# Performance work log

Measured on AMD Instinct MI355X. Metric: run time of the kernel, lower is better.

The kernel has to match this reference:

```python
import jax, jax.numpy as jnp
import numpy as np

T, B, D, H, O = 512, 64, 256, 1024, 64
DT = 0.1
TAU_MIN, TAU_MAX = 0.01, 1.0
DZDT_MAX, Z_MAX = 10.0, 100.0


def setup_inputs() -> dict:
    key = jax.random.key(0)
    ks = jax.random.split(key, 9)
    sc = lambda k, shape, s: (jax.random.normal(k, shape, jnp.float32) * s)
    return {
        "x": jax.random.normal(ks[0], (T, B, D), jnp.float32),
        # recurrent weights (torch Linear stores [out, in]; y = x @ W.T)
        "W_real": sc(ks[1], (H, H), 0.03),
        "W_imag": sc(ks[2], (H, H), 0.03),
        "U_w": sc(ks[3], (H, D), 0.06),
        "U_b": jnp.zeros((H,), jnp.float32),
        "W_tau_w": sc(ks[4], (H, H), 0.01),
        "W_tau_b": jnp.zeros((H,), jnp.float32),
        # sparse mask logits (module applies sigmoid to these params at fwd time)
        "mask_real": jax.random.normal(ks[5], (H, H), jnp.float32),
        "mask_imag": jax.random.normal(ks[6], (H, H), jnp.float32),
        "tau_bias": jnp.zeros((H,), jnp.float32),
        "b_real": jnp.zeros((H,), jnp.float32),
        "b_imag": jnp.zeros((H,), jnp.float32),
        "out_w": sc(ks[7], (O, H), 0.03),
        "out_b": jnp.zeros((O,), jnp.float32),
    }


def reference(x, W_real, W_imag, U_w, U_b, W_tau_w, W_tau_b,
              mask_real, mask_imag, tau_bias, b_real, b_imag, out_w, out_b):
    # Masked recurrent weights are constant over time: fold sigmoid(mask) once.
    Wr = W_real * jax.nn.sigmoid(mask_real)  # [H,H]
    Wi = W_imag * jax.nn.sigmoid(mask_imag)  # [H,H]
    # Input drive U(x_t) is the same for real and imag parts; precompute for all t.
    Ux = jnp.einsum('tbd,hd->tbh', x, U_w) + U_b  # [T,B,H]

    def step(z, ux):
        zr, zi = z  # complex state as (real, imag), each [B,H]
        dz_r = -zr + jnp.tanh(zr) @ Wr.T + ux + b_real
        dz_i = -zi + jnp.tanh(zi) @ Wi.T + ux + b_imag
        # tau gate from |z| (1e-20 keeps sqrt grad finite at z=0, value unchanged)
        z_mod = jnp.sqrt(zr * zr + zi * zi + 1e-20)
        tau = jax.nn.sigmoid(z_mod @ W_tau_w.T + W_tau_b) + tau_bias
        tau = jnp.clip(tau, TAU_MIN, TAU_MAX) + 1e-6
        dzr = jnp.clip(dz_r / tau, -DZDT_MAX, DZDT_MAX)
        dzi = jnp.clip(dz_i / tau, -DZDT_MAX, DZDT_MAX)
        zr = jnp.clip(zr + DT * dzr, -Z_MAX, Z_MAX)
        zi = jnp.clip(zi + DT * dzi, -Z_MAX, Z_MAX)
        y = zr @ out_w.T + out_b  # readout on real part, [B,O]
        return (zr, zi), y

    z0 = (jnp.zeros((B, H), x.dtype), jnp.zeros((B, H), x.dtype))
    _, ys = jax.lax.scan(step, z0, Ux)
    return ys  # [T,B,O]
```

## Files before the change

### kernel.cpp

```cpp
#include <hip/hip_runtime.h>

static constexpr int TT = 512, BBATCH = 64, DD = 256, HH = 1024, OOUT = 64;

typedef float f32x4 __attribute__((ext_vector_type(4)));
typedef short bfrag __attribute__((ext_vector_type(8)));

__device__ __forceinline__ float sigm(float x) { return 1.0f / (1.0f + __expf(-x)); }
__device__ __forceinline__ float tanh_fast(float x) {
    return 1.0f - 2.0f / (__expf(2.0f * x) + 1.0f);
}
__device__ __forceinline__ unsigned short f2bf(float f) {
    unsigned int u = __builtin_bit_cast(unsigned int, f);
    u += 0x7FFFu + ((u >> 16) & 1u);
    return (unsigned short)(u >> 16);
}

struct Params {
    const float *x, *W_real, *W_imag, *U_w, *U_b, *W_tau_w, *W_tau_b,
                *mask_real, *mask_imag, *tau_bias, *b_real, *b_imag, *out_w, *out_b;
    float* out;
    unsigned short* act;
    float* zread;
    unsigned int* bar;
};

#define LDC(v_, p_, o_) asm volatile("global_load_dwordx4 %0, %1, off offset:" #o_ " sc0 sc1" \
                                     : "=v"(v_) : "v"(p_))
#define WAITV(n_) do { asm volatile("s_waitcnt vmcnt(" #n_ ")" ::: "memory"); \
                       __builtin_amdgcn_sched_barrier(0); } while (0)
#define MFMA(a_, b_, c_) __builtin_amdgcn_mfma_f32_16x16x32_bf16(a_, b_, c_, 0, 0, 0)
#define STC(p_, v_) __hip_atomic_store((p_), (v_), __ATOMIC_RELAXED, __HIP_MEMORY_SCOPE_AGENT)

__global__ void __launch_bounds__(512, 2) lnn_fused(Params p) {
    extern __shared__ char smem[];
    unsigned short* Wlds = (unsigned short*)smem;
    unsigned short* Ulds = (unsigned short*)(smem + 3 * 16 * 1024 * 2);
    float* EX = (float*)(smem + 3 * 16 * 1024 * 2 + 16 * 256 * 2);

    const int tid = threadIdx.x;
    const int wave = tid >> 6, lane = tid & 63;
    const int g = blockIdx.x;
    const int grp = (g & 7) >> 1;
    const int slot = ((g >> 3) << 1) | (g & 1);
    const int h0 = slot * 16, b0 = grp * 16;
    const int ro_b0 = b0 + (slot & 3) * 4, ro_o0 = (slot >> 2) * 4;

    for (int i = tid; i < 3 * 16 * 1024; i += 512) {
        const int mat = i >> 14, r = (i >> 10) & 15, k = i & 1023;
        const int idx = (h0 + r) * HH + k;
        float w;
        if (mat == 0)      w = p.W_real[idx] * sigm(p.mask_real[idx]);
        else if (mat == 1) w = p.W_imag[idx] * sigm(p.mask_imag[idx]);
        else               w = p.W_tau_w[idx];
        const int gk = (k >> 3) ^ (r & 7);
        Wlds[(mat * 16 + r) * 1024 + gk * 8 + (k & 7)] = f2bf(w);
    }
    for (int i = tid; i < 16 * 256; i += 512) {
        const int r = i >> 8, k = i & 255;
        const int gk = (k >> 3) ^ (r & 7);
        Ulds[r * 256 + gk * 8 + (k & 7)] = f2bf(p.U_w[(h0 + r) * DD + k]);
    }

    float zr = 0.f, zi = 0.f, cbr = 0.f, cbi = 0.f, cwtb = 0.f, ctb = 0.f, cub = 0.f;
    int myoff = 0;
    if (tid < 256) {
        const int myb = b0 + (tid >> 4), myh = h0 + (tid & 15);
        myoff = myb * HH + myh;
        cbr = p.b_real[myh]; cbi = p.b_imag[myh];
        cwtb = p.W_tau_b[myh]; ctb = p.tau_bias[myh]; cub = p.U_b[myh];
        STC(p.act + (0 * 2 + 1) * BBATCH * HH + myoff, (unsigned short)0);
        STC(p.act + (1 * 2 + 1) * BBATCH * HH + myoff, (unsigned short)0);
        STC(p.act + (2 * 2 + 1) * BBATCH * HH + myoff, (unsigned short)0);
    }

    unsigned int* bar = p.bar + grp * 32;
    auto group_barrier = [&](unsigned int gen) {
        __syncthreads();
        if (tid == 0) {
            __hip_atomic_fetch_add(bar, 1u, __ATOMIC_RELAXED, __HIP_MEMORY_SCOPE_AGENT);
            const unsigned int tgt = 64u * gen;
            int guard = 1 << 20;
            while (__hip_atomic_load(bar, __ATOMIC_RELAXED, __HIP_MEMORY_SCOPE_AGENT) < tgt
                   && --guard)
                __builtin_amdgcn_s_sleep(1);
        }
        __syncthreads();
    };

    group_barrier(1);

    for (int t = 0; t <= TT; ++t) {
        const int rp = (t + 1) & 1;
        const int wp2 = t & 1;

        if (t < TT && wave < 6) {
            const int mat = wave >> 1, half = wave & 1;
            const int m = lane & 15, kb = lane >> 4, sw = m & 7;
            const unsigned short* aptr = p.act + (mat * 2 + rp) * BBATCH * HH
                                         + (b0 + m) * HH + half * 512 + kb * 8;
            bfrag a0,a1,a2,a3,a4,a5,a6,a7,a8,a9,a10,a11,a12,a13,a14,a15;
            LDC(a0,aptr,0);    LDC(a1,aptr,64);   LDC(a2,aptr,128);  LDC(a3,aptr,192);
            LDC(a4,aptr,256);  LDC(a5,aptr,320);  LDC(a6,aptr,384);  LDC(a7,aptr,448);
            LDC(a8,aptr,512);  LDC(a9,aptr,576);  LDC(a10,aptr,640); LDC(a11,aptr,704);
            LDC(a12,aptr,768); LDC(a13,aptr,832); LDC(a14,aptr,896); LDC(a15,aptr,960);
            f32x4 acc = {0.f, 0.f, 0.f, 0.f};
            const unsigned short* wrow = Wlds + (mat * 16 + m) * 1024;
            #define STW(ks_, av_) acc = MFMA(av_, *(const bfrag*)(wrow + \
                ((((half << 6) + ((ks_) << 2) + kb) ^ sw) << 3)), acc);
            WAITV(8);
            STW(0,a0) STW(1,a1) STW(2,a2) STW(3,a3)
            STW(4,a4) STW(5,a5) STW(6,a6) STW(7,a7)
            WAITV(0);
            STW(8,a8) STW(9,a9) STW(10,a10) STW(11,a11)
            STW(12,a12) STW(13,a13) STW(14,a14) STW(15,a15)
            #undef STW
            #pragma unroll
            for (int q = 0; q < 4; ++q)
                EX[wave * 256 + (kb * 4 + q) * 16 + m] = acc[q];
        } else if (wave == 6 && t < TT) {
            const int m = lane & 15, kb = lane >> 4, sw = m & 7;
            const float* xrow = p.x + ((size_t)t * BBATCH + (b0 + m)) * DD;
            const unsigned short* urow = Ulds + m * 256;
            f32x4 acc = {0.f, 0.f, 0.f, 0.f};
            #pragma unroll
            for (int ks = 0; ks < 8; ++ks) {
                const int k = ks * 32 + kb * 8;
                const f32x4 x0 = *(const f32x4*)(xrow + k);
                const f32x4 x1 = *(const f32x4*)(xrow + k + 4);
                bfrag a;
                a[0]=(short)f2bf(x0[0]); a[1]=(short)f2bf(x0[1]);
                a[2]=(short)f2bf(x0[2]); a[3]=(short)f2bf(x0[3]);
                a[4]=(short)f2bf(x1[0]); a[5]=(short)f2bf(x1[1]);
                a[6]=(short)f2bf(x1[2]); a[7]=(short)f2bf(x1[3]);
                const bfrag b = *(const bfrag*)(urow + (((ks * 4 + kb) ^ sw) << 3));
                acc = MFMA(a, b, acc);
            }
            #pragma unroll
            for (int q = 0; q < 4; ++q)
                EX[6 * 256 + (kb * 4 + q) * 16 + m] = acc[q];
        } else if (wave == 7 && t >= 1) {
            const int r = lane & 15, kq = lane >> 4;
            const int bb = ro_b0 + (r >> 2), oo = ro_o0 + (r & 3);
            const float* zp = p.zread + ((t - 1) & 1) * BBATCH * HH + bb * HH + kq * 256;
            const float* owp = p.out_w + oo * HH + kq * 256;
            float acc = 0.f;
            #define RB(bt_) { \
                const float* zq = zp + (bt_) * 64; \
                f32x4 z0,z1,z2,z3,z4,z5,z6,z7,z8,z9,z10,z11,z12,z13,z14,z15; \
                LDC(z0,zq,0);    LDC(z1,zq,16);   LDC(z2,zq,32);   LDC(z3,zq,48); \
                LDC(z4,zq,64);   LDC(z5,zq,80);   LDC(z6,zq,96);   LDC(z7,zq,112); \
                LDC(z8,zq,128);  LDC(z9,zq,144);  LDC(z10,zq,160); LDC(z11,zq,176); \
                LDC(z12,zq,192); LDC(z13,zq,208); LDC(z14,zq,224); LDC(z15,zq,240); \
                WAITV(0); \
                const f32x4* wq = (const f32x4*)(owp + (bt_) * 64); \
                acc += z0[0]*wq[0][0]+z0[1]*wq[0][1]+z0[2]*wq[0][2]+z0[3]*wq[0][3]; \
                acc += z1[0]*wq[1][0]+z1[1]*wq[1][1]+z1[2]*wq[1][2]+z1[3]*wq[1][3]; \
                acc += z2[0]*wq[2][0]+z2[1]*wq[2][1]+z2[2]*wq[2][2]+z2[3]*wq[2][3]; \
                acc += z3[0]*wq[3][0]+z3[1]*wq[3][1]+z3[2]*wq[3][2]+z3[3]*wq[3][3]; \
                acc += z4[0]*wq[4][0]+z4[1]*wq[4][1]+z4[2]*wq[4][2]+z4[3]*wq[4][3]; \
                acc += z5[0]*wq[5][0]+z5[1]*wq[5][1]+z5[2]*wq[5][2]+z5[3]*wq[5][3]; \
                acc += z6[0]*wq[6][0]+z6[1]*wq[6][1]+z6[2]*wq[6][2]+z6[3]*wq[6][3]; \
                acc += z7[0]*wq[7][0]+z7[1]*wq[7][1]+z7[2]*wq[7][2]+z7[3]*wq[7][3]; \
                acc += z8[0]*wq[8][0]+z8[1]*wq[8][1]+z8[2]*wq[8][2]+z8[3]*wq[8][3]; \
                acc += z9[0]*wq[9][0]+z9[1]*wq[9][1]+z9[2]*wq[9][2]+z9[3]*wq[9][3]; \
                acc += z10[0]*wq[10][0]+z10[1]*wq[10][1]+z10[2]*wq[10][2]+z10[3]*wq[10][3]; \
                acc += z11[0]*wq[11][0]+z11[1]*wq[11][1]+z11[2]*wq[11][2]+z11[3]*wq[11][3]; \
                acc += z12[0]*wq[12][0]+z12[1]*wq[12][1]+z12[2]*wq[12][2]+z12[3]*wq[12][3]; \
                acc += z13[0]*wq[13][0]+z13[1]*wq[13][1]+z13[2]*wq[13][2]+z13[3]*wq[13][3]; \
                acc += z14[0]*wq[14][0]+z14[1]*wq[14][1]+z14[2]*wq[14][2]+z14[3]*wq[14][3]; \
                acc += z15[0]*wq[15][0]+z15[1]*wq[15][1]+z15[2]*wq[15][2]+z15[3]*wq[15][3]; }
            RB(0) RB(1) RB(2) RB(3)
            #undef RB
            acc += __shfl_xor(acc, 16, 64);
            acc += __shfl_xor(acc, 32, 64);
            if (kq == 0)
                p.out[(size_t)(t - 1) * BBATCH * OOUT + bb * OOUT + oo] = acc + p.out_b[oo];
        }

        __syncthreads();

        if (t < TT && tid < 256) {
            const float mr = EX[0 * 256 + tid] + EX[1 * 256 + tid];
            const float mi = EX[2 * 256 + tid] + EX[3 * 256 + tid];
            const float mt = EX[4 * 256 + tid] + EX[5 * 256 + tid];
            const float ux = EX[6 * 256 + tid] + cub;
            const float dr0 = -zr + mr + ux + cbr;
            const float di0 = -zi + mi + ux + cbi;
            float tau = sigm(mt + cwtb) + ctb;
            tau = fminf(fmaxf(tau, 0.01f), 1.0f) + 1e-6f;
            const float dzr = fminf(fmaxf(dr0 / tau, -10.f), 10.f);
            const float dzi = fminf(fmaxf(di0 / tau, -10.f), 10.f);
            zr = fminf(fmaxf(zr + 0.1f * dzr, -100.f), 100.f);
            zi = fminf(fmaxf(zi + 0.1f * dzi, -100.f), 100.f);
            const float ar = tanh_fast(zr), ai = tanh_fast(zi);
            const float zm = sqrtf(zr * zr + zi * zi + 1e-20f);
            STC(p.act + (0 * 2 + wp2) * BBATCH * HH + myoff, f2bf(ar));
            STC(p.act + (1 * 2 + wp2) * BBATCH * HH + myoff, f2bf(ai));
            STC(p.act + (2 * 2 + wp2) * BBATCH * HH + myoff, f2bf(zm));
            STC(p.zread + wp2 * BBATCH * HH + myoff, zr);
        }

        if (t < TT) group_barrier(t + 2);
    }
}

extern "C" void kernel_launch(void* const* d_in, const int* in_sizes, int n_in,
                              void* d_out, int out_size, void* d_ws, size_t ws_size,
                              hipStream_t stream) {
    Params p;
    p.x         = (const float*)d_in[0];
    p.W_real    = (const float*)d_in[1];
    p.W_imag    = (const float*)d_in[2];
    p.U_w       = (const float*)d_in[3];
    p.U_b       = (const float*)d_in[4];
    p.W_tau_w   = (const float*)d_in[5];
    p.W_tau_b   = (const float*)d_in[6];
    p.mask_real = (const float*)d_in[7];
    p.mask_imag = (const float*)d_in[8];
    p.tau_bias  = (const float*)d_in[9];
    p.b_real    = (const float*)d_in[10];
    p.b_imag    = (const float*)d_in[11];
    p.out_w     = (const float*)d_in[12];
    p.out_b     = (const float*)d_in[13];
    p.out   = (float*)d_out;
    p.act   = (unsigned short*)d_ws;
    p.zread = (float*)((char*)d_ws + 786432);
    p.bar   = (unsigned int*)((char*)d_ws + 1310720);

    hipMemsetAsync((char*)d_ws + 1310720, 0, 512, stream);

    constexpr unsigned smem = 3 * 16 * 1024 * 2 + 16 * 256 * 2 + 8 * 256 * 4;
    hipFuncSetAttribute(reinterpret_cast<const void*>(lnn_fused),
                        hipFuncAttributeMaxDynamicSharedMemorySize, smem);
    void* args[] = { &p };
    hipLaunchCooperativeKernel(reinterpret_cast<const void*>(lnn_fused),
                               dim3(256), dim3(512), args, smem, stream);
}
```

Measured before the change: 5.110 ms.

## Add XCD-local partitioned kernel with L2-coherent exchange and fallback path

```diff
diff --git a/kernel.cpp b/kernel.cpp
--- a/kernel.cpp
+++ b/kernel.cpp
@@ -21,17 +21,370 @@
     float* out;
     unsigned short* act;
     float* zread;
-    unsigned int* bar;
+    unsigned int* ctr;
+    unsigned int* xccmap;
+    unsigned short* uslab;
+    unsigned short* wtau;
+    int haveWT;
 };
 
+#define LDL(v_, p_, o_) asm volatile("global_load_dwordx4 %0, %1, off offset:" #o_ " sc0" \
+                                     : "=v"(v_) : "v"(p_))
 #define LDC(v_, p_, o_) asm volatile("global_load_dwordx4 %0, %1, off offset:" #o_ " sc0 sc1" \
+                                     : "=v"(v_) : "v"(p_))
+#define LDP(v_, p_, o_) asm volatile("global_load_dwordx4 %0, %1, off offset:" #o_ \
                                      : "=v"(v_) : "v"(p_))
 #define WAITV(n_) do { asm volatile("s_waitcnt vmcnt(" #n_ ")" ::: "memory"); \
                        __builtin_amdgcn_sched_barrier(0); } while (0)
 #define MFMA(a_, b_, c_) __builtin_amdgcn_mfma_f32_16x16x32_bf16(a_, b_, c_, 0, 0, 0)
 #define STC(p_, v_) __hip_atomic_store((p_), (v_), __ATOMIC_RELAXED, __HIP_MEMORY_SCOPE_AGENT)
 
-__global__ void __launch_bounds__(512, 2) lnn_fused(Params p) {
+#define ISSUE_A16(MACRO_) do { \
+    MACRO_(a0,ap,0);   MACRO_(a1,ap,64);  MACRO_(a2,ap,128);  MACRO_(a3,ap,192);  \
+    MACRO_(a4,ap,256); MACRO_(a5,ap,320); MACRO_(a6,ap,384);  MACRO_(a7,ap,448);  \
+    MACRO_(a8,ap,512); MACRO_(a9,ap,576); MACRO_(a10,ap,640); MACRO_(a11,ap,704); \
+    MACRO_(a12,ap,768);MACRO_(a13,ap,832);MACRO_(a14,ap,896); MACRO_(a15,ap,960); } while (0)
+
+__global__ void __launch_bounds__(512, 2) lnn_xcd(Params p) {
+    extern __shared__ char smem[];
+    unsigned short* Wlds = (unsigned short*)smem;
+    float* EX = (float*)(smem + 131072);
+    __shared__ int sh_mode;
+
+    const int tid = threadIdx.x, wave = tid >> 6, lane = tid & 63;
+    const int g = blockIdx.x, grp = g & 7, slot = g >> 3;
+    const int h0 = slot * 32, b0g = grp * 8;
+    const int gact = grp * 49152;
+    const int gz = grp * 16384;
+
+    for (int i = tid; i < 2 * 32 * 1024; i += 512) {
+        const int mat = i >> 15, r = (i >> 10) & 31, k = i & 1023;
+        const int idx = (h0 + r) * HH + k;
+        const float w = (mat == 0) ? p.W_real[idx] * sigm(p.mask_real[idx])
+                                   : p.W_imag[idx] * sigm(p.mask_imag[idx]);
+        const int gk = (k >> 3) ^ (r & 7);
+        Wlds[(mat * 32 + r) * 1024 + gk * 8 + (k & 7)] = f2bf(w);
+    }
+    if (tid == 0) {
+        unsigned int x;
+        asm volatile("s_getreg_b32 %0, hwreg(HW_REG_XCC_ID)" : "=s"(x));
+        p.xccmap[g] = x & 15u;
+    }
+    if (p.haveWT && grp == 0) {
+        for (int e = tid; e < 4096; e += 512) {
+            const int ks = e & 15, l = (e >> 4) & 63, kh = (e >> 10) & 1, tle = e >> 11;
+            const int m = l & 15, kb = l >> 4;
+            const float* s = p.W_tau_w + (size_t)(h0 + tle * 16 + m) * HH
+                             + kh * 512 + ks * 32 + kb * 8;
+            unsigned short* d = p.wtau + (size_t)slot * 32768 + e * 8;
+            #pragma unroll
+            for (int j = 0; j < 8; ++j) d[j] = f2bf(s[j]);
+        }
+        for (int e = tid; e < 1024; e += 512) {
+            const int ks = e & 7, l = (e >> 3) & 63, tle = e >> 9;
+            const int m = l & 15, kb = l >> 4;
+            const float* s = p.U_w + (size_t)(h0 + tle * 16 + m) * DD + ks * 32 + kb * 8;
+            unsigned short* d = p.uslab + (size_t)slot * 8192 + e * 8;
+            #pragma unroll
+            for (int j = 0; j < 8; ++j) d[j] = f2bf(s[j]);
+        }
+    }
+    __syncthreads();
+    if (tid == 0) __threadfence();
+    __syncthreads();
+    if (tid == 0) {
+        __hip_atomic_fetch_add(p.ctr, 1u, __ATOMIC_RELAXED, __HIP_MEMORY_SCOPE_AGENT);
+        int guard = 1 << 18;
+        while (__hip_atomic_load(p.ctr, __ATOMIC_RELAXED, __HIP_MEMORY_SCOPE_AGENT) < 256u
+               && --guard)
+            __builtin_amdgcn_s_sleep(1);
+        unsigned int x0 = 0; int ok = 1;
+        for (int j = 0; j < 32; ++j) {
+            const unsigned int* q = p.xccmap + (grp + 8 * j);
+            unsigned int v;
+            asm volatile("global_load_dword %0, %1, off sc0 sc1\n\ts_waitcnt vmcnt(0)"
+                         : "=v"(v) : "v"(q) : "memory");
+            if (j == 0) x0 = v; else ok &= (v == x0);
+        }
+        sh_mode = ok;
+    }
+    __syncthreads();
+    const int lm = sh_mode;
+
+    float zr = 0.f, zi = 0.f, cbr = 0.f, cbi = 0.f, cwtb = 0.f, ctb = 0.f, cub = 0.f;
+    int myoff = 0;
+    if (tid < 256) {
+        const int myb = tid >> 5, mh = tid & 31, hh = h0 + mh;
+        myoff = myb * 1024 + hh;
+        cbr = p.b_real[hh]; cbi = p.b_imag[hh];
+        cwtb = p.W_tau_b[hh]; ctb = p.tau_bias[hh]; cub = p.U_b[hh];
+        if (lm) {
+            p.act[gact + 1 * 8192 + myoff] = 0;
+            p.act[gact + 3 * 8192 + myoff] = 0;
+            p.act[gact + 5 * 8192 + myoff] = 0;
+        } else {
+            STC(p.act + gact + 1 * 8192 + myoff, (unsigned short)0);
+            STC(p.act + gact + 3 * 8192 + myoff, (unsigned short)0);
+            STC(p.act + gact + 5 * 8192 + myoff, (unsigned short)0);
+        }
+    }
+
+    unsigned int* bar = p.ctr + 32 + grp * 32;
+    auto gbar = [&](unsigned int gen) {
+        __syncthreads();
+        if (tid == 0) {
+            const unsigned int tgt = 32u * gen;
+            if (lm) {
+                asm volatile("global_atomic_add %0, %1, off" :: "v"(bar), "v"(1u) : "memory");
+                unsigned int v; int guard = 1 << 18;
+                do {
+                    __builtin_amdgcn_s_sleep(1);
+                    asm volatile("global_load_dword %0, %1, off sc0\n\ts_waitcnt vmcnt(0)"
+                                 : "=v"(v) : "v"(bar) : "memory");
+                } while (v < tgt && --guard);
+            } else {
+                __hip_atomic_fetch_add(bar, 1u, __ATOMIC_RELAXED, __HIP_MEMORY_SCOPE_AGENT);
+                int guard = 1 << 18;
+                while (__hip_atomic_load(bar, __ATOMIC_RELAXED, __HIP_MEMORY_SCOPE_AGENT) < tgt
+                       && --guard)
+                    __builtin_amdgcn_s_sleep(1);
+            }
+        }
+        __syncthreads();
+    };
+
+    gbar(1);
+
+    for (int t = 0; t <= TT; ++t) {
+        const int rp = (t + 1) & 1;
+
+        if (t < TT && wave < 4) {
+            const int mat = wave >> 1, kh = wave & 1;
+            const int m = lane & 15, kb = lane >> 4, sw = m & 7;
+            const unsigned short* ap = p.act + gact + (mat * 2 + rp) * 8192
+                                       + (m & 7) * 1024 + kh * 512 + kb * 8;
+            bfrag a0,a1,a2,a3,a4,a5,a6,a7,a8,a9,a10,a11,a12,a13,a14,a15;
+            if (lm) ISSUE_A16(LDL); else ISSUE_A16(LDC);
+            f32x4 acc0 = {0.f,0.f,0.f,0.f}, acc1 = {0.f,0.f,0.f,0.f};
+            const unsigned short* w0 = Wlds + (mat * 32 + m) * 1024;
+            const unsigned short* w1 = w0 + 16 * 1024;
+            #define ST2(ks_, av_) { const int gi = ((kh * 16 + (ks_)) * 4 + kb) ^ sw; \
+                acc0 = MFMA(av_, *(const bfrag*)(w0 + (gi << 3)), acc0); \
+                acc1 = MFMA(av_, *(const bfrag*)(w1 + (gi << 3)), acc1); }
+            WAITV(8);
+            ST2(0,a0) ST2(1,a1) ST2(2,a2) ST2(3,a3)
+            ST2(4,a4) ST2(5,a5) ST2(6,a6) ST2(7,a7)
+            WAITV(0);
+            ST2(8,a8) ST2(9,a9) ST2(10,a10) ST2(11,a11)
+            ST2(12,a12) ST2(13,a13) ST2(14,a14) ST2(15,a15)
+            #undef ST2
+            if (kb < 2) {
+                float* e0 = EX + ((mat * 2 + kh) * 2) * 128;
+                #pragma unroll
+                for (int q = 0; q < 4; ++q) {
+                    e0[(kb * 4 + q) * 16 + m] = acc0[q];
+                    e0[128 + (kb * 4 + q) * 16 + m] = acc1[q];
+                }
+            }
+        } else if (t < TT && wave < 6) {
+            const int kh = wave & 1;
+            const int m = lane & 15, kb = lane >> 4;
+            const unsigned short* ap = p.act + gact + (4 + rp) * 8192
+                                       + (m & 7) * 1024 + kh * 512 + kb * 8;
+            bfrag a0,a1,a2,a3,a4,a5,a6,a7,a8,a9,a10,a11,a12,a13,a14,a15;
+            if (lm) ISSUE_A16(LDL); else ISSUE_A16(LDC);
+            f32x4 acc0 = {0.f,0.f,0.f,0.f}, acc1 = {0.f,0.f,0.f,0.f};
+            if (p.haveWT) {
+                const unsigned short* wb = p.wtau + (size_t)slot * 32768;
+                const unsigned short* bp0 = wb + ((size_t)((0 * 2 + kh) * 64 + lane)) * 128;
+                const unsigned short* bp1 = wb + ((size_t)((1 * 2 + kh) * 64 + lane)) * 128;
+                bfrag b0,b1,b2,b3,b4,b5,b6,b7,b8,b9,b10,b11,b12,b13,b14,b15;
+                #define ISSUE_B16(bp_) do { \
+                    LDP(b0,bp_,0);   LDP(b1,bp_,16);  LDP(b2,bp_,32);   LDP(b3,bp_,48);  \
+                    LDP(b4,bp_,64);  LDP(b5,bp_,80);  LDP(b6,bp_,96);   LDP(b7,bp_,112); \
+                    LDP(b8,bp_,128); LDP(b9,bp_,144); LDP(b10,bp_,160); LDP(b11,bp_,176);\
+                    LDP(b12,bp_,192);LDP(b13,bp_,208);LDP(b14,bp_,224); LDP(b15,bp_,240);} while (0)
+                #define MF16(acc_) { \
+                    acc_ = MFMA(a0,b0,acc_);   acc_ = MFMA(a1,b1,acc_); \
+                    acc_ = MFMA(a2,b2,acc_);   acc_ = MFMA(a3,b3,acc_); \
+                    acc_ = MFMA(a4,b4,acc_);   acc_ = MFMA(a5,b5,acc_); \
+                    acc_ = MFMA(a6,b6,acc_);   acc_ = MFMA(a7,b7,acc_); \
+                    acc_ = MFMA(a8,b8,acc_);   acc_ = MFMA(a9,b9,acc_); \
+                    acc_ = MFMA(a10,b10,acc_); acc_ = MFMA(a11,b11,acc_); \
+                    acc_ = MFMA(a12,b12,acc_); acc_ = MFMA(a13,b13,acc_); \
+                    acc_ = MFMA(a14,b14,acc_); acc_ = MFMA(a15,b15,acc_); }
+                ISSUE_B16(bp0);
+                WAITV(0);
+                MF16(acc0);
+                ISSUE_B16(bp1);
+                WAITV(0);
+                MF16(acc1);
+                #undef MF16
+                #undef ISSUE_B16
+            } else {
+                WAITV(0);
+                const float* q0 = p.W_tau_w + (size_t)(h0 + m) * HH + kh * 512 + kb * 8;
+                const float* q1 = q0 + 16 * HH;
+                #define MFS(ks_, av_) { \
+                    const f32x4 u0 = *(const f32x4*)(q0 + (ks_) * 32); \
+                    const f32x4 u1 = *(const f32x4*)(q0 + (ks_) * 32 + 4); \
+                    const f32x4 v0 = *(const f32x4*)(q1 + (ks_) * 32); \
+                    const f32x4 v1 = *(const f32x4*)(q1 + (ks_) * 32 + 4); \
+                    bfrag bb0, bb1; \
+                    bb0[0]=(short)f2bf(u0[0]); bb0[1]=(short)f2bf(u0[1]); \
+                    bb0[2]=(short)f2bf(u0[2]); bb0[3]=(short)f2bf(u0[3]); \
+                    bb0[4]=(short)f2bf(u1[0]); bb0[5]=(short)f2bf(u1[1]); \
+                    bb0[6]=(short)f2bf(u1[2]); bb0[7]=(short)f2bf(u1[3]); \
+                    bb1[0]=(short)f2bf(v0[0]); bb1[1]=(short)f2bf(v0[1]); \
+                    bb1[2]=(short)f2bf(v0[2]); bb1[3]=(short)f2bf(v0[3]); \
+                    bb1[4]=(short)f2bf(v1[0]); bb1[5]=(short)f2bf(v1[1]); \
+                    bb1[6]=(short)f2bf(v1[2]); bb1[7]=(short)f2bf(v1[3]); \
+                    acc0 = MFMA(av_, bb0, acc0); acc1 = MFMA(av_, bb1, acc1); }
+                MFS(0,a0) MFS(1,a1) MFS(2,a2) MFS(3,a3)
+                MFS(4,a4) MFS(5,a5) MFS(6,a6) MFS(7,a7)
+                MFS(8,a8) MFS(9,a9) MFS(10,a10) MFS(11,a11)
+                MFS(12,a12) MFS(13,a13) MFS(14,a14) MFS(15,a15)
+                #undef MFS
+            }
+            if (kb < 2) {
+                float* e0 = EX + ((4 + kh) * 2) * 128;
+                #pragma unroll
+                for (int q = 0; q < 4; ++q) {
+                    e0[(kb * 4 + q) * 16 + m] = acc0[q];
+                    e0[128 + (kb * 4 + q) * 16 + m] = acc1[q];
+                }
+            }
+        } else if (wave == 6 && t < TT) {
+            const int m = lane & 15, kb = lane >> 4;
+            const float* xrow = p.x + ((size_t)t * BBATCH + b0g + (m & 7)) * DD + kb * 8;
+            f32x4 acc0 = {0.f,0.f,0.f,0.f}, acc1 = {0.f,0.f,0.f,0.f};
+            if (p.haveWT) {
+                const bfrag* u0 = (const bfrag*)(p.uslab + (size_t)slot * 8192) + lane * 8;
+                const bfrag* u1 = u0 + 64 * 8;
+                #pragma unroll
+                for (int ks = 0; ks < 8; ++ks) {
+                    const f32x4 x0 = *(const f32x4*)(xrow + ks * 32);
+                    const f32x4 x1 = *(const f32x4*)(xrow + ks * 32 + 4);
+                    bfrag a;
+                    a[0]=(short)f2bf(x0[0]); a[1]=(short)f2bf(x0[1]);
+                    a[2]=(short)f2bf(x0[2]); a[3]=(short)f2bf(x0[3]);
+                    a[4]=(short)f2bf(x1[0]); a[5]=(short)f2bf(x1[1]);
+                    a[6]=(short)f2bf(x1[2]); a[7]=(short)f2bf(x1[3]);
+                    acc0 = MFMA(a, u0[ks], acc0);
+                    acc1 = MFMA(a, u1[ks], acc1);
+                }
+            } else {
+                const float* q0 = p.U_w + (size_t)(h0 + m) * DD + kb * 8;
+                const float* q1 = q0 + 16 * DD;
+                #pragma unroll
+                for (int ks = 0; ks < 8; ++ks) {
+                    const f32x4 x0 = *(const f32x4*)(xrow + ks * 32);
+                    const f32x4 x1 = *(const f32x4*)(xrow + ks * 32 + 4);
+                    const f32x4 u0 = *(const f32x4*)(q0 + ks * 32);
+                    const f32x4 u1 = *(const f32x4*)(q0 + ks * 32 + 4);
+                    const f32x4 v0 = *(const f32x4*)(q1 + ks * 32);
+                    const f32x4 v1 = *(const f32x4*)(q1 + ks * 32 + 4);
+                    bfrag a, bb0, bb1;
+                    a[0]=(short)f2bf(x0[0]); a[1]=(short)f2bf(x0[1]);
+                    a[2]=(short)f2bf(x0[2]); a[3]=(short)f2bf(x0[3]);
+                    a[4]=(short)f2bf(x1[0]); a[5]=(short)f2bf(x1[1]);
+                    a[6]=(short)f2bf(x1[2]); a[7]=(short)f2bf(x1[3]);
+                    bb0[0]=(short)f2bf(u0[0]); bb0[1]=(short)f2bf(u0[1]);
+                    bb0[2]=(short)f2bf(u0[2]); bb0[3]=(short)f2bf(u0[3]);
+                    bb0[4]=(short)f2bf(u1[0]); bb0[5]=(short)f2bf(u1[1]);
+                    bb0[6]=(short)f2bf(u1[2]); bb0[7]=(short)f2bf(u1[3]);
+                    bb1[0]=(short)f2bf(v0[0]); bb1[1]=(short)f2bf(v0[1]);
+                    bb1[2]=(short)f2bf(v0[2]); bb1[3]=(short)f2bf(v0[3]);
+                    bb1[4]=(short)f2bf(v1[0]); bb1[5]=(short)f2bf(v1[1]);
+                    bb1[6]=(short)f2bf(v1[2]); bb1[7]=(short)f2bf(v1[3]);
+                    acc0 = MFMA(a, bb0, acc0);
+                    acc1 = MFMA(a, bb1, acc1);
+                }
+            }
+            if (kb < 2) {
+                #pragma unroll
+                for (int q = 0; q < 4; ++q) {
+                    EX[12 * 128 + (kb * 4 + q) * 16 + m] = acc0[q];
+                    EX[13 * 128 + (kb * 4 + q) * 16 + m] = acc1[q];
+                }
+            }
+        } else if (wave == 7 && t >= 1) {
+            const int b = lane >> 3, kc = lane & 7, o0 = slot * 2;
+            const float* zp = p.zread + gz + ((t - 1) & 1) * 8192 + b * 1024 + kc * 128;
+            const float* w0 = p.out_w + (size_t)o0 * HH + kc * 128;
+            const float* w1 = w0 + HH;
+            float s0 = 0.f, s1 = 0.f;
+            #pragma unroll
+            for (int hf = 0; hf < 2; ++hf) {
+                const float* zq = zp + hf * 64;
+                f32x4 z0,z1,z2,z3,z4,z5,z6,z7,z8,z9,z10,z11,z12,z13,z14,z15;
+                if (lm) {
+                    LDL(z0,zq,0);    LDL(z1,zq,16);   LDL(z2,zq,32);   LDL(z3,zq,48);
+                    LDL(z4,zq,64);   LDL(z5,zq,80);   LDL(z6,zq,96);   LDL(z7,zq,112);
+                    LDL(z8,zq,128);  LDL(z9,zq,144);  LDL(z10,zq,160); LDL(z11,zq,176);
+                    LDL(z12,zq,192); LDL(z13,zq,208); LDL(z14,zq,224); LDL(z15,zq,240);
+                } else {
+                    LDC(z0,zq,0);    LDC(z1,zq,16);   LDC(z2,zq,32);   LDC(z3,zq,48);
+                    LDC(z4,zq,64);   LDC(z5,zq,80);   LDC(z6,zq,96);   LDC(z7,zq,112);
+                    LDC(z8,zq,128);  LDC(z9,zq,144);  LDC(z10,zq,160); LDC(z11,zq,176);
+                    LDC(z12,zq,192); LDC(z13,zq,208); LDC(z14,zq,224); LDC(z15,zq,240);
+                }
+                WAITV(0);
+                const f32x4* a0 = (const f32x4*)(w0 + hf * 64);
+                const f32x4* a1 = (const f32x4*)(w1 + hf * 64);
+                #define DOT(zi_, i_) { \
+                    s0 += zi_[0]*a0[i_][0]+zi_[1]*a0[i_][1]+zi_[2]*a0[i_][2]+zi_[3]*a0[i_][3]; \
+                    s1 += zi_[0]*a1[i_][0]+zi_[1]*a1[i_][1]+zi_[2]*a1[i_][2]+zi_[3]*a1[i_][3]; }
+                DOT(z0,0) DOT(z1,1) DOT(z2,2) DOT(z3,3) DOT(z4,4) DOT(z5,5) DOT(z6,6) DOT(z7,7)
+                DOT(z8,8) DOT(z9,9) DOT(z10,10) DOT(z11,11) DOT(z12,12) DOT(z13,13) DOT(z14,14) DOT(z15,15)
+                #undef DOT
+            }
+            s0 += __shfl_xor(s0, 1, 64); s1 += __shfl_xor(s1, 1, 64);
+            s0 += __shfl_xor(s0, 2, 64); s1 += __shfl_xor(s1, 2, 64);
+            s0 += __shfl_xor(s0, 4, 64); s1 += __shfl_xor(s1, 4, 64);
+            if (kc == 0) {
+                float2 y = { s0 + p.out_b[o0], s1 + p.out_b[o0 + 1] };
+                *(float2*)(p.out + (size_t)(t - 1) * BBATCH * OOUT + (b0g + b) * OOUT + o0) = y;
+            }
+        }
+
+        __syncthreads();
+
+        if (t < TT && tid < 256) {
+            const int mh = tid & 31, tle = mh >> 4, ii = (tid >> 5) * 16 + (mh & 15);
+            const float mr = EX[(0 + tle) * 128 + ii] + EX[(2 + tle) * 128 + ii];
+            const float mi = EX[(4 + tle) * 128 + ii] + EX[(6 + tle) * 128 + ii];
+            const float mt = EX[(8 + tle) * 128 + ii] + EX[(10 + tle) * 128 + ii];
+            const float ux = EX[(12 + tle) * 128 + ii] + cub;
+            const float dr0 = -zr + mr + ux + cbr;
+            const float di0 = -zi + mi + ux + cbi;
+            float tau = sigm(mt + cwtb) + ctb;
+            tau = fminf(fmaxf(tau, 0.01f), 1.0f) + 1e-6f;
+            const float dzr = fminf(fmaxf(dr0 / tau, -10.f), 10.f);
+            const float dzi = fminf(fmaxf(di0 / tau, -10.f), 10.f);
+            zr = fminf(fmaxf(zr + 0.1f * dzr, -100.f), 100.f);
+            zi = fminf(fmaxf(zi + 0.1f * dzi, -100.f), 100.f);
+            const float ar = tanh_fast(zr), ai = tanh_fast(zi);
+            const float zm = sqrtf(zr * zr + zi * zi + 1e-20f);
+            const int wp2 = t & 1;
+            if (lm) {
+                p.act[gact + (0 + wp2) * 8192 + myoff] = f2bf(ar);
+                p.act[gact + (2 + wp2) * 8192 + myoff] = f2bf(ai);
+                p.act[gact + (4 + wp2) * 8192 + myoff] = f2bf(zm);
+                p.zread[gz + wp2 * 8192 + myoff] = zr;
+            } else {
+                STC(p.act + gact + (0 + wp2) * 8192 + myoff, f2bf(ar));
+                STC(p.act + gact + (2 + wp2) * 8192 + myoff, f2bf(ai));
+                STC(p.act + gact + (4 + wp2) * 8192 + myoff, f2bf(zm));
+                STC(p.zread + gz + wp2 * 8192 + myoff, zr);
+            }
+        }
+
+        if (t < TT) gbar(t + 2);
+    }
+}
+
+__global__ void __launch_bounds__(512, 2) lnn_llc(Params p) {
     extern __shared__ char smem[];
     unsigned short* Wlds = (unsigned short*)smem;
     unsigned short* Ulds = (unsigned short*)(smem + 3 * 16 * 1024 * 2);
@@ -73,7 +426,7 @@
         STC(p.act + (2 * 2 + 1) * BBATCH * HH + myoff, (unsigned short)0);
     }
 
-    unsigned int* bar = p.bar + grp * 32;
+    unsigned int* bar = p.ctr + 32 + grp * 32;
     auto group_barrier = [&](unsigned int gen) {
         __syncthreads();
         if (tid == 0) {
@@ -96,13 +449,10 @@
         if (t < TT && wave < 6) {
             const int mat = wave >> 1, half = wave & 1;
             const int m = lane & 15, kb = lane >> 4, sw = m & 7;
-            const unsigned short* aptr = p.act + (mat * 2 + rp) * BBATCH * HH
-                                         + (b0 + m) * HH + half * 512 + kb * 8;
+            const unsigned short* ap = p.act + (mat * 2 + rp) * BBATCH * HH
+                                       + (b0 + m) * HH + half * 512 + kb * 8;
             bfrag a0,a1,a2,a3,a4,a5,a6,a7,a8,a9,a10,a11,a12,a13,a14,a15;
-            LDC(a0,aptr,0);    LDC(a1,aptr,64);   LDC(a2,aptr,128);  LDC(a3,aptr,192);
-            LDC(a4,aptr,256);  LDC(a5,aptr,320);  LDC(a6,aptr,384);  LDC(a7,aptr,448);
-            LDC(a8,aptr,512);  LDC(a9,aptr,576);  LDC(a10,aptr,640); LDC(a11,aptr,704);
-            LDC(a12,aptr,768); LDC(a13,aptr,832); LDC(a14,aptr,896); LDC(a15,aptr,960);
+            ISSUE_A16(LDC);
             f32x4 acc = {0.f, 0.f, 0.f, 0.f};
             const unsigned short* wrow = Wlds + (mat * 16 + m) * 1024;
             #define STW(ks_, av_) acc = MFMA(av_, *(const bfrag*)(wrow + \
@@ -222,17 +572,35 @@
     p.b_imag    = (const float*)d_in[11];
     p.out_w     = (const float*)d_in[12];
     p.out_b     = (const float*)d_in[13];
-    p.out   = (float*)d_out;
-    p.act   = (unsigned short*)d_ws;
-    p.zread = (float*)((char*)d_ws + 786432);
-    p.bar   = (unsigned int*)((char*)d_ws + 1310720);
-
-    hipMemsetAsync((char*)d_ws + 1310720, 0, 512, stream);
-
-    constexpr unsigned smem = 3 * 16 * 1024 * 2 + 16 * 256 * 2 + 8 * 256 * 4;
-    hipFuncSetAttribute(reinterpret_cast<const void*>(lnn_fused),
-                        hipFuncAttributeMaxDynamicSharedMemorySize, smem);
+    p.out    = (float*)d_out;
+    p.act    = (unsigned short*)d_ws;
+    p.zread  = (float*)((char*)d_ws + 786432);
+    p.ctr    = (unsigned int*)((char*)d_ws + 1310720);
+    p.xccmap = (unsigned int*)((char*)d_ws + 1312768);
+    p.uslab  = (unsigned short*)((char*)d_ws + 1313792);
+    p.wtau   = (unsigned short*)((char*)d_ws + 1838080);
+    p.haveWT = (ws_size >= (size_t)1838080 + 2097152) ? 1 : 0;
+
+    hipMemsetAsync((char*)d_ws + 1310720, 0, 3072, stream);
+
+    constexpr unsigned SMX = 131072 + 14 * 128 * 4;
+    constexpr unsigned SML = 3 * 16 * 1024 * 2 + 16 * 256 * 2 + 8 * 256 * 4;
     void* args[] = { &p };
-    hipLaunchCooperativeKernel(reinterpret_cast<const void*>(lnn_fused),
-                               dim3(256), dim3(512), args, smem, stream);
+
+    int nb = 0;
+    hipError_t ea = hipFuncSetAttribute(reinterpret_cast<const void*>(lnn_xcd),
+                                        hipFuncAttributeMaxDynamicSharedMemorySize, SMX);
+    hipOccupancyMaxActiveBlocksPerMultiprocessor(&nb, reinterpret_cast<const void*>(lnn_xcd),
+                                                 512, SMX);
+    hipError_t el = hipErrorUnknown;
+    if (ea == hipSuccess && nb >= 1)
+        el = hipLaunchCooperativeKernel(reinterpret_cast<const void*>(lnn_xcd),
+                                        dim3(256), dim3(512), args, SMX, stream);
+    if (el != hipSuccess) {
+        (void)hipGetLastError();
+        hipFuncSetAttribute(reinterpret_cast<const void*>(lnn_llc),
+                            hipFuncAttributeMaxDynamicSharedMemorySize, SML);
+        hipLaunchCooperativeKernel(reinterpret_cast<const void*>(lnn_llc),
+                                   dim3(256), dim3(512), args, SML, stream);
+    }
 }
```

Result: no change. 5.118 ms (+0.2%).

## Split group barrier into arrive/wait and overlap Ux and readout inside it

Applied to the files above, without the earlier changes.

```diff
diff --git a/kernel.cpp b/kernel.cpp
--- a/kernel.cpp
+++ b/kernel.cpp
@@ -74,35 +74,106 @@
     }
 
     unsigned int* bar = p.bar + grp * 32;
-    auto group_barrier = [&](unsigned int gen) {
-        __syncthreads();
-        if (tid == 0) {
-            __hip_atomic_fetch_add(bar, 1u, __ATOMIC_RELAXED, __HIP_MEMORY_SCOPE_AGENT);
-            const unsigned int tgt = 64u * gen;
-            int guard = 1 << 20;
-            while (__hip_atomic_load(bar, __ATOMIC_RELAXED, __HIP_MEMORY_SCOPE_AGENT) < tgt
-                   && --guard)
-                __builtin_amdgcn_s_sleep(1);
+    auto arrive = [&]() {
+        __hip_atomic_fetch_add(bar, 1u, __ATOMIC_RELAXED, __HIP_MEMORY_SCOPE_AGENT);
+    };
+    auto waitbar = [&](unsigned int tgt) {
+        int guard = 1 << 20;
+        while (__hip_atomic_load(bar, __ATOMIC_RELAXED, __HIP_MEMORY_SCOPE_AGENT) < tgt
+               && --guard)
+            __builtin_amdgcn_s_sleep(1);
+    };
+
+    auto uxcomp = [&](int tx) {
+        const int m = lane & 15, kb = lane >> 4, sw = m & 7;
+        const float* xrow = p.x + ((size_t)tx * BBATCH + (b0 + m)) * DD;
+        const unsigned short* urow = Ulds + m * 256;
+        f32x4 acc = {0.f, 0.f, 0.f, 0.f};
+        #pragma unroll
+        for (int ks = 0; ks < 8; ++ks) {
+            const int k = ks * 32 + kb * 8;
+            const f32x4 x0 = *(const f32x4*)(xrow + k);
+            const f32x4 x1 = *(const f32x4*)(xrow + k + 4);
+            bfrag a;
+            a[0]=(short)f2bf(x0[0]); a[1]=(short)f2bf(x0[1]);
+            a[2]=(short)f2bf(x0[2]); a[3]=(short)f2bf(x0[3]);
+            a[4]=(short)f2bf(x1[0]); a[5]=(short)f2bf(x1[1]);
+            a[6]=(short)f2bf(x1[2]); a[7]=(short)f2bf(x1[3]);
+            const bfrag b = *(const bfrag*)(urow + (((ks * 4 + kb) ^ sw) << 3));
+            acc = MFMA(a, b, acc);
         }
-        __syncthreads();
-    };
-
-    group_barrier(1);
-
-    for (int t = 0; t <= TT; ++t) {
+        float* e = EX + (6 + (tx & 1)) * 256;
+        #pragma unroll
+        for (int q = 0; q < 4; ++q)
+            e[(kb * 4 + q) * 16 + m] = acc[q];
+    };
+    auto readout = [&](int ty) {
+        const int r = lane & 15, kq = lane >> 4;
+        const int bb = ro_b0 + (r >> 2), oo = ro_o0 + (r & 3);
+        const float* zp = p.zread + (ty & 1) * BBATCH * HH + bb * HH + kq * 256;
+        const float* owp = p.out_w + oo * HH + kq * 256;
+        float acc = 0.f;
+        f32x4 A0,A1,A2,A3,A4,A5,A6,A7,A8,A9,A10,A11,A12,A13,A14,A15;
+        f32x4 B0,B1,B2,B3,B4,B5,B6,B7,B8,B9,B10,B11,B12,B13,B14,B15;
+        #define ISSUE_BANK(P_, zq_) do { \
+            LDC(P_##0,zq_,0);    LDC(P_##1,zq_,16);   LDC(P_##2,zq_,32);   LDC(P_##3,zq_,48);  \
+            LDC(P_##4,zq_,64);   LDC(P_##5,zq_,80);   LDC(P_##6,zq_,96);   LDC(P_##7,zq_,112); \
+            LDC(P_##8,zq_,128);  LDC(P_##9,zq_,144);  LDC(P_##10,zq_,160); LDC(P_##11,zq_,176);\
+            LDC(P_##12,zq_,192); LDC(P_##13,zq_,208); LDC(P_##14,zq_,224); LDC(P_##15,zq_,240);} while (0)
+        #define DOT_BANK(P_, wq_) do { const f32x4* wq = (const f32x4*)(wq_); \
+            acc += P_##0[0]*wq[0][0]+P_##0[1]*wq[0][1]+P_##0[2]*wq[0][2]+P_##0[3]*wq[0][3]; \
+            acc += P_##1[0]*wq[1][0]+P_##1[1]*wq[1][1]+P_##1[2]*wq[1][2]+P_##1[3]*wq[1][3]; \
+            acc += P_##2[0]*wq[2][0]+P_##2[1]*wq[2][1]+P_##2[2]*wq[2][2]+P_##2[3]*wq[2][3]; \
+            acc += P_##3[0]*wq[3][0]+P_##3[1]*wq[3][1]+P_##3[2]*wq[3][2]+P_##3[3]*wq[3][3]; \
+            acc += P_##4[0]*wq[4][0]+P_##4[1]*wq[4][1]+P_##4[2]*wq[4][2]+P_##4[3]*wq[4][3]; \
+            acc += P_##5[0]*wq[5][0]+P_##5[1]*wq[5][1]+P_##5[2]*wq[5][2]+P_##5[3]*wq[5][3]; \
+            acc += P_##6[0]*wq[6][0]+P_##6[1]*wq[6][1]+P_##6[2]*wq[6][2]+P_##6[3]*wq[6][3]; \
+            acc += P_##7[0]*wq[7][0]+P_##7[1]*wq[7][1]+P_##7[2]*wq[7][2]+P_##7[3]*wq[7][3]; \
+            acc += P_##8[0]*wq[8][0]+P_##8[1]*wq[8][1]+P_##8[2]*wq[8][2]+P_##8[3]*wq[8][3]; \
+            acc += P_##9[0]*wq[9][0]+P_##9[1]*wq[9][1]+P_##9[2]*wq[9][2]+P_##9[3]*wq[9][3]; \
+            acc += P_##10[0]*wq[10][0]+P_##10[1]*wq[10][1]+P_##10[2]*wq[10][2]+P_##10[3]*wq[10][3]; \
+            acc += P_##11[0]*wq[11][0]+P_##11[1]*wq[11][1]+P_##11[2]*wq[11][2]+P_##11[3]*wq[11][3]; \
+            acc += P_##12[0]*wq[12][0]+P_##12[1]*wq[12][1]+P_##12[2]*wq[12][2]+P_##12[3]*wq[12][3]; \
+            acc += P_##13[0]*wq[13][0]+P_##13[1]*wq[13][1]+P_##13[2]*wq[13][2]+P_##13[3]*wq[13][3]; \
+            acc += P_##14[0]*wq[14][0]+P_##14[1]*wq[14][1]+P_##14[2]*wq[14][2]+P_##14[3]*wq[14][3]; \
+            acc += P_##15[0]*wq[15][0]+P_##15[1]*wq[15][1]+P_##15[2]*wq[15][2]+P_##15[3]*wq[15][3]; } while (0)
+        ISSUE_BANK(A, (zp));
+        ISSUE_BANK(B, (zp + 64));
+        WAITV(16); DOT_BANK(A, owp);
+        ISSUE_BANK(A, (zp + 128));
+        WAITV(16); DOT_BANK(B, owp + 64);
+        ISSUE_BANK(B, (zp + 192));
+        WAITV(16); DOT_BANK(A, owp + 128);
+        WAITV(0);  DOT_BANK(B, owp + 192);
+        #undef ISSUE_BANK
+        #undef DOT_BANK
+        acc += __shfl_xor(acc, 16, 64);
+        acc += __shfl_xor(acc, 32, 64);
+        if (kq == 0)
+            p.out[(size_t)ty * BBATCH * OOUT + bb * OOUT + oo] = acc + p.out_b[oo];
+    };
+
+    __syncthreads();
+    if (wave == 6) uxcomp(0);
+
+    __syncthreads();
+    if (tid == 0) { arrive(); waitbar(64u); }
+    __syncthreads();
+
+    for (int t = 0; t < TT; ++t) {
         const int rp = (t + 1) & 1;
-        const int wp2 = t & 1;
-
-        if (t < TT && wave < 6) {
+        const int wp = t & 1;
+
+        if (wave < 6) {
             const int mat = wave >> 1, half = wave & 1;
             const int m = lane & 15, kb = lane >> 4, sw = m & 7;
-            const unsigned short* aptr = p.act + (mat * 2 + rp) * BBATCH * HH
-                                         + (b0 + m) * HH + half * 512 + kb * 8;
+            const unsigned short* ap = p.act + (mat * 2 + rp) * BBATCH * HH
+                                       + (b0 + m) * HH + half * 512 + kb * 8;
             bfrag a0,a1,a2,a3,a4,a5,a6,a7,a8,a9,a10,a11,a12,a13,a14,a15;
-            LDC(a0,aptr,0);    LDC(a1,aptr,64);   LDC(a2,aptr,128);  LDC(a3,aptr,192);
-            LDC(a4,aptr,256);  LDC(a5,aptr,320);  LDC(a6,aptr,384);  LDC(a7,aptr,448);
-            LDC(a8,aptr,512);  LDC(a9,aptr,576);  LDC(a10,aptr,640); LDC(a11,aptr,704);
-            LDC(a12,aptr,768); LDC(a13,aptr,832); LDC(a14,aptr,896); LDC(a15,aptr,960);
+            LDC(a0,ap,0);    LDC(a1,ap,64);   LDC(a2,ap,128);  LDC(a3,ap,192);
+            LDC(a4,ap,256);  LDC(a5,ap,320);  LDC(a6,ap,384);  LDC(a7,ap,448);
+            LDC(a8,ap,512);  LDC(a9,ap,576);  LDC(a10,ap,640); LDC(a11,ap,704);
+            LDC(a12,ap,768); LDC(a13,ap,832); LDC(a14,ap,896); LDC(a15,ap,960);
             f32x4 acc = {0.f, 0.f, 0.f, 0.f};
             const unsigned short* wrow = Wlds + (mat * 16 + m) * 1024;
             #define STW(ks_, av_) acc = MFMA(av_, *(const bfrag*)(wrow + \
@@ -117,73 +188,15 @@
             #pragma unroll
             for (int q = 0; q < 4; ++q)
                 EX[wave * 256 + (kb * 4 + q) * 16 + m] = acc[q];
-        } else if (wave == 6 && t < TT) {
-            const int m = lane & 15, kb = lane >> 4, sw = m & 7;
-            const float* xrow = p.x + ((size_t)t * BBATCH + (b0 + m)) * DD;
-            const unsigned short* urow = Ulds + m * 256;
-            f32x4 acc = {0.f, 0.f, 0.f, 0.f};
-            #pragma unroll
-            for (int ks = 0; ks < 8; ++ks) {
-                const int k = ks * 32 + kb * 8;
-                const f32x4 x0 = *(const f32x4*)(xrow + k);
-                const f32x4 x1 = *(const f32x4*)(xrow + k + 4);
-                bfrag a;
-                a[0]=(short)f2bf(x0[0]); a[1]=(short)f2bf(x0[1]);
-                a[2]=(short)f2bf(x0[2]); a[3]=(short)f2bf(x0[3]);
-                a[4]=(short)f2bf(x1[0]); a[5]=(short)f2bf(x1[1]);
-                a[6]=(short)f2bf(x1[2]); a[7]=(short)f2bf(x1[3]);
-                const bfrag b = *(const bfrag*)(urow + (((ks * 4 + kb) ^ sw) << 3));
-                acc = MFMA(a, b, acc);
-            }
-            #pragma unroll
-            for (int q = 0; q < 4; ++q)
-                EX[6 * 256 + (kb * 4 + q) * 16 + m] = acc[q];
-        } else if (wave == 7 && t >= 1) {
-            const int r = lane & 15, kq = lane >> 4;
-            const int bb = ro_b0 + (r >> 2), oo = ro_o0 + (r & 3);
-            const float* zp = p.zread + ((t - 1) & 1) * BBATCH * HH + bb * HH + kq * 256;
-            const float* owp = p.out_w + oo * HH + kq * 256;
-            float acc = 0.f;
-            #define RB(bt_) { \
-                const float* zq = zp + (bt_) * 64; \
-                f32x4 z0,z1,z2,z3,z4,z5,z6,z7,z8,z9,z10,z11,z12,z13,z14,z15; \
-                LDC(z0,zq,0);    LDC(z1,zq,16);   LDC(z2,zq,32);   LDC(z3,zq,48); \
-                LDC(z4,zq,64);   LDC(z5,zq,80);   LDC(z6,zq,96);   LDC(z7,zq,112); \
-                LDC(z8,zq,128);  LDC(z9,zq,144);  LDC(z10,zq,160); LDC(z11,zq,176); \
-                LDC(z12,zq,192); LDC(z13,zq,208); LDC(z14,zq,224); LDC(z15,zq,240); \
-                WAITV(0); \
-                const f32x4* wq = (const f32x4*)(owp + (bt_) * 64); \
-                acc += z0[0]*wq[0][0]+z0[1]*wq[0][1]+z0[2]*wq[0][2]+z0[3]*wq[0][3]; \
-                acc += z1[0]*wq[1][0]+z1[1]*wq[1][1]+z1[2]*wq[1][2]+z1[3]*wq[1][3]; \
-                acc += z2[0]*wq[2][0]+z2[1]*wq[2][1]+z2[2]*wq[2][2]+z2[3]*wq[2][3]; \
-                acc += z3[0]*wq[3][0]+z3[1]*wq[3][1]+z3[2]*wq[3][2]+z3[3]*wq[3][3]; \
-                acc += z4[0]*wq[4][0]+z4[1]*wq[4][1]+z4[2]*wq[4][2]+z4[3]*wq[4][3]; \
-                acc += z5[0]*wq[5][0]+z5[1]*wq[5][1]+z5[2]*wq[5][2]+z5[3]*wq[5][3]; \
-                acc += z6[0]*wq[6][0]+z6[1]*wq[6][1]+z6[2]*wq[6][2]+z6[3]*wq[6][3]; \
-                acc += z7[0]*wq[7][0]+z7[1]*wq[7][1]+z7[2]*wq[7][2]+z7[3]*wq[7][3]; \
-                acc += z8[0]*wq[8][0]+z8[1]*wq[8][1]+z8[2]*wq[8][2]+z8[3]*wq[8][3]; \
-                acc += z9[0]*wq[9][0]+z9[1]*wq[9][1]+z9[2]*wq[9][2]+z9[3]*wq[9][3]; \
-                acc += z10[0]*wq[10][0]+z10[1]*wq[10][1]+z10[2]*wq[10][2]+z10[3]*wq[10][3]; \
-                acc += z11[0]*wq[11][0]+z11[1]*wq[11][1]+z11[2]*wq[11][2]+z11[3]*wq[11][3]; \
-                acc += z12[0]*wq[12][0]+z12[1]*wq[12][1]+z12[2]*wq[12][2]+z12[3]*wq[12][3]; \
-                acc += z13[0]*wq[13][0]+z13[1]*wq[13][1]+z13[2]*wq[13][2]+z13[3]*wq[13][3]; \
-                acc += z14[0]*wq[14][0]+z14[1]*wq[14][1]+z14[2]*wq[14][2]+z14[3]*wq[14][3]; \
-                acc += z15[0]*wq[15][0]+z15[1]*wq[15][1]+z15[2]*wq[15][2]+z15[3]*wq[15][3]; }
-            RB(0) RB(1) RB(2) RB(3)
-            #undef RB
-            acc += __shfl_xor(acc, 16, 64);
-            acc += __shfl_xor(acc, 32, 64);
-            if (kq == 0)
-                p.out[(size_t)(t - 1) * BBATCH * OOUT + bb * OOUT + oo] = acc + p.out_b[oo];
         }
 
         __syncthreads();
 
-        if (t < TT && tid < 256) {
+        if (tid < 256) {
             const float mr = EX[0 * 256 + tid] + EX[1 * 256 + tid];
             const float mi = EX[2 * 256 + tid] + EX[3 * 256 + tid];
             const float mt = EX[4 * 256 + tid] + EX[5 * 256 + tid];
-            const float ux = EX[6 * 256 + tid] + cub;
+            const float ux = EX[(6 + (t & 1)) * 256 + tid] + cub;
             const float dr0 = -zr + mr + ux + cbr;
             const float di0 = -zi + mi + ux + cbi;
             float tau = sigm(mt + cwtb) + ctb;
@@ -194,14 +207,21 @@
             zi = fminf(fmaxf(zi + 0.1f * dzi, -100.f), 100.f);
             const float ar = tanh_fast(zr), ai = tanh_fast(zi);
             const float zm = sqrtf(zr * zr + zi * zi + 1e-20f);
-            STC(p.act + (0 * 2 + wp2) * BBATCH * HH + myoff, f2bf(ar));
-            STC(p.act + (1 * 2 + wp2) * BBATCH * HH + myoff, f2bf(ai));
-            STC(p.act + (2 * 2 + wp2) * BBATCH * HH + myoff, f2bf(zm));
-            STC(p.zread + wp2 * BBATCH * HH + myoff, zr);
+            STC(p.act + (0 * 2 + wp) * BBATCH * HH + myoff, f2bf(ar));
+            STC(p.act + (1 * 2 + wp) * BBATCH * HH + myoff, f2bf(ai));
+            STC(p.act + (2 * 2 + wp) * BBATCH * HH + myoff, f2bf(zm));
+            STC(p.zread + wp * BBATCH * HH + myoff, zr);
         }
 
-        if (t < TT) group_barrier(t + 2);
-    }
+        __syncthreads();
+        if (tid == 0) arrive();
+        if (wave == 6 && t + 1 < TT) uxcomp(t + 1);
+        if (wave == 7 && t >= 1) readout(t - 1);
+        if (tid == 0) waitbar(64u * (t + 2));
+        __syncthreads();
+    }
+
+    if (wave == 7) readout(TT - 1);
 }
 
 extern "C" void kernel_launch(void* const* d_in, const int* in_sizes, int n_in,
```

Measured after the change: 5.001 ms. 2.1% less time.
